# Kernel optimization log

Measured on AMD Instinct MI355X. Metric: run time of the kernel, lower is better.

Reference implementation:

```python
import jax, jax.numpy as jnp
import numpy as np

N_NODES = 100000
N_EDGES = 3200000
D_IN = 128
D_OUT = 128


def setup_inputs() -> dict:
    key = jax.random.key(0)
    k1, k2, k3 = jax.random.split(key, 3)
    x = jax.random.normal(k1, (N_NODES, D_IN), dtype=jnp.float32)
    edge_index = jax.random.randint(k2, (2, N_EDGES), 0, N_NODES, dtype=jnp.int64)
    # Glorot-style init for the GCN linear weight [out, in]
    weight = jax.random.normal(k3, (D_OUT, D_IN), dtype=jnp.float32) * (1.0 / np.sqrt(D_IN))
    bias = jnp.zeros((D_OUT,), dtype=jnp.float32)
    return {"x": x, "edge_index": edge_index, "weight": weight, "bias": bias}


def reference(x, edge_index, weight, bias):
    """LinearEncoder.forward: (GCNConv(x, edge_index), 0).

    GCNConv: out = D^-1/2 (A + I) D^-1/2 (x W^T) + b  (symmetric norm, self-loops).
    """
    n = x.shape[0]
    src = edge_index[0]
    dst = edge_index[1]
    # add self-loops
    loops = jnp.arange(n, dtype=src.dtype)
    src = jnp.concatenate([src, loops])
    dst = jnp.concatenate([dst, loops])
    # degree (in-degree over destination nodes, unit edge weights)
    ones = jnp.ones(src.shape[0], dtype=x.dtype)
    deg = jax.ops.segment_sum(ones, dst, num_segments=n)
    deg_inv_sqrt = jnp.where(deg > 0, jax.lax.rsqrt(deg), 0.0).astype(x.dtype)
    norm = deg_inv_sqrt[src] * deg_inv_sqrt[dst]  # [E+N]
    # dense transform first (as in PyG GCNConv), then sparse aggregation
    h = x @ weight.T  # [N, D_OUT]
    msgs = h[src] * norm[:, None]  # [E+N, D_OUT]
    out = jax.ops.segment_sum(msgs, dst, num_segments=n) + bias
    return (out, 0)
```

## Files before the change

### kernel.cpp

```cpp
#include <hip/hip_runtime.h>
#include <hip/hip_bf16.h>

#define N_NODES 100000
#define N_EDGES 3200000
#define D 128

typedef unsigned short u16;

#define BKT_W 512
#define NBKT 196
#define NSH 8
#define CAPS 2304
#define CAPB (NSH * CAPS)
#define EPB 5120
#define P1B 625
#define EPT 20

#define CW_BLOCKS 2

typedef __attribute__((ext_vector_type(8))) short bf16x8;
typedef __attribute__((ext_vector_type(4))) float f32x4;

__device__ __forceinline__ float bf2f(u16 u) {
    union { unsigned i; float f; } a; a.i = ((unsigned)u) << 16; return a.f;
}
__device__ __forceinline__ float asf(unsigned u) {
    union { unsigned i; float f; } a; a.i = u; return a.f;
}
__device__ __forceinline__ u16 f2bf(float f) {
    __hip_bfloat16 b = __float2bfloat16(f);
    return *(u16*)&b;
}

__global__ __launch_bounds__(256) void p1_multisplit(const int* __restrict__ ei,
                                                     int* __restrict__ bcnt,
                                                     unsigned* __restrict__ bbuf) {
    __shared__ unsigned s1[EPB];
    __shared__ unsigned s2[EPB];
    __shared__ int hist[NBKT], lbase[NBKT], cur[NBKT], gbase[NBKT];
    __shared__ int wsum4[4], wbase4[4];
    int t = threadIdx.x, blk = blockIdx.x;
    int sh = blk & (NSH - 1);
    int e0 = blk * EPB;
    if (t < NBKT) hist[t] = 0;
    __syncthreads();

    unsigned char bk[EPT];
#pragma unroll
    for (int k = 0; k < EPT; ++k) {
        int i = k * 256 + t;
        int s = ei[e0 + i];
        int d = ei[N_EDGES + e0 + i];
        unsigned bkt = (unsigned)d >> 9;
        bk[k] = (unsigned char)bkt;
        s1[i] = ((unsigned)s << 9) | ((unsigned)d & 511u);
        atomicAdd(&hist[bkt], 1);
    }
    __syncthreads();

    if (t < NBKT) gbase[t] = atomicAdd(&bcnt[t * NSH + sh], hist[t]);

    int lane = t & 63, wv = t >> 6;
    int hv = (t < NBKT) ? hist[t] : 0;
    int pre = hv;
#pragma unroll
    for (int o = 1; o < 64; o <<= 1) {
        int u = __shfl_up(pre, o);
        if (lane >= o) pre += u;
    }
    if (lane == 63) wsum4[wv] = pre;
    __syncthreads();
    if (t == 0) {
        int b = 0;
#pragma unroll
        for (int k = 0; k < 4; ++k) { wbase4[k] = b; b += wsum4[k]; }
    }
    __syncthreads();
    if (t < NBKT) { int ex = wbase4[wv] + pre - hv; lbase[t] = ex; cur[t] = ex; }
    __syncthreads();

#pragma unroll
    for (int k = 0; k < EPT; ++k) {
        int i = k * 256 + t;
        int p = atomicAdd(&cur[bk[k]], 1);
        s2[p] = s1[i];
    }
    __syncthreads();

    for (int bkt = wv; bkt < NBKT; bkt += 4) {
        int n = hist[bkt], lb = lbase[bkt], gb = gbase[bkt];
        unsigned* dst = bbuf + ((size_t)bkt * NSH + sh) * CAPS;
        for (int j = lane; j < n; j += 64) {
            int p = gb + j;
            if (p < CAPS) dst[p] = s2[lb + j];
        }
    }
}

__global__ __launch_bounds__(1024) void p2_localsort(const unsigned* __restrict__ bbuf,
                                                     const int* __restrict__ bcnt,
                                                     int* __restrict__ sorted,
                                                     int* __restrict__ beg_g,
                                                     int* __restrict__ cnt_g,
                                                     float* __restrict__ dinv_g,
                                                     const float* __restrict__ w,
                                                     u16* __restrict__ wbf) {
    __shared__ int hist[BKT_W], cur[BKT_W], shcnt[NSH];
    __shared__ int wsum[8], wbase[8];
    int b = blockIdx.x, t = threadIdx.x;

    if (b >= NBKT) {
        int idx = (b - NBKT) * 1024 + t;
        const float4* wp = (const float4*)(w + (size_t)idx * 8);
        float4 a = wp[0], bb = wp[1];
        union { u16 h[8]; uint4 v; } o;
        o.h[0] = f2bf(a.x); o.h[1] = f2bf(a.y);
        o.h[2] = f2bf(a.z); o.h[3] = f2bf(a.w);
        o.h[4] = f2bf(bb.x); o.h[5] = f2bf(bb.y);
        o.h[6] = f2bf(bb.z); o.h[7] = f2bf(bb.w);
        ((uint4*)wbf)[idx] = o.v;
        return;
    }

    if (t < NSH) { int m = bcnt[b * NSH + t]; shcnt[t] = m > CAPS ? CAPS : m; }
    if (t < BKT_W) hist[t] = 0;
    __syncthreads();

    for (int sh = 0; sh < NSH; ++sh) {
        int m = shcnt[sh];
        const unsigned* p = bbuf + ((size_t)b * NSH + sh) * CAPS;
        for (int i = t; i < m; i += 1024) atomicAdd(&hist[p[i] & 511u], 1);
    }
    __syncthreads();

    int lane = t & 63, wv = t >> 6;
    int hv = (t < BKT_W) ? hist[t] : 0;
    int pre = hv;
#pragma unroll
    for (int o = 1; o < 64; o <<= 1) {
        int u = __shfl_up(pre, o);
        if (lane >= o) pre += u;
    }
    if (wv < 8 && lane == 63) wsum[wv] = pre;
    __syncthreads();
    if (wv == 0) {
        int v = (lane < 8) ? wsum[lane] : 0;
        int pp = v;
#pragma unroll
        for (int o = 1; o < 8; o <<= 1) {
            int u = __shfl_up(pp, o);
            if (lane >= o) pp += u;
        }
        if (lane < 8) wbase[lane] = pp - v;
    }
    __syncthreads();
    int ex = 0;
    if (t < BKT_W) { ex = wbase[wv] + pre - hv; cur[t] = ex; }

    if (t < BKT_W) {
        int node = b * BKT_W + t;
        if (node < N_NODES) {
            cnt_g[node] = hv;
            beg_g[node] = b * CAPB + ex;
            dinv_g[node] = rsqrtf((float)(hv + 1));
        }
    }
    __syncthreads();

    int* dst = sorted + (size_t)b * CAPB;
    for (int sh = 0; sh < NSH; ++sh) {
        int m = shcnt[sh];
        const unsigned* p = bbuf + ((size_t)b * NSH + sh) * CAPS;
        for (int i = t; i < m; i += 1024) {
            unsigned ww = p[i];
            int pp = atomicAdd(&cur[ww & 511u], 1);
            dst[pp] = (int)(ww >> 9);
        }
    }
}

__global__ __launch_bounds__(256) void gemm_h(const float* __restrict__ x,
                                              const u16* __restrict__ wbf,
                                              const float* __restrict__ dinv,
                                              u16* __restrict__ h) {
    int t = threadIdx.x;
    int wave = t >> 6, lane = t & 63;
    int n0 = blockIdx.x * 64 + wave * 16;
    int lrow = lane & 15;
    int quad = lane >> 4;

    int arow = n0 + lrow;
    const float* ap = x + (size_t)(arow < N_NODES ? arow : 0) * D;
    bf16x8 afrag[4];
#pragma unroll
    for (int kt = 0; kt < 4; ++kt) {
        int k0 = kt * 32 + quad * 8;
        f32x4 x0 = *(const f32x4*)(ap + k0);
        f32x4 x1 = *(const f32x4*)(ap + k0 + 4);
        bf16x8 a;
        a[0] = (short)f2bf(x0.x); a[1] = (short)f2bf(x0.y);
        a[2] = (short)f2bf(x0.z); a[3] = (short)f2bf(x0.w);
        a[4] = (short)f2bf(x1.x); a[5] = (short)f2bf(x1.y);
        a[6] = (short)f2bf(x1.z); a[7] = (short)f2bf(x1.w);
        afrag[kt] = a;
    }

    float dsc[4];
#pragma unroll
    for (int i = 0; i < 4; ++i) {
        int n = n0 + quad * 4 + i;
        dsc[i] = (n < N_NODES) ? dinv[n] : 0.f;
    }

#pragma unroll
    for (int jt = 0; jt < 8; ++jt) {
        int j0 = jt * 16;
        f32x4 acc = {0.f, 0.f, 0.f, 0.f};
#pragma unroll
        for (int kt = 0; kt < 4; ++kt) {
            int k0 = kt * 32 + quad * 8;
            bf16x8 b = *(const bf16x8*)(wbf + (size_t)(j0 + lrow) * D + k0);
            acc = __builtin_amdgcn_mfma_f32_16x16x32_bf16(afrag[kt], b, acc, 0, 0, 0);
        }
#pragma unroll
        for (int i = 0; i < 4; ++i) {
            int n = n0 + quad * 4 + i;
            if (n < N_NODES) h[(size_t)n * D + j0 + lrow] = f2bf(acc[i] * dsc[i]);
        }
    }
}

__global__ __launch_bounds__(256) void aggregate_h(const u16* __restrict__ h,
                                                   const float* __restrict__ dinv,
                                                   const int* __restrict__ beg_g,
                                                   const int* __restrict__ cnt_g,
                                                   const int* __restrict__ sorted_src,
                                                   const float* __restrict__ bias,
                                                   float* __restrict__ out) {
    int w = threadIdx.x >> 6;
    int l = threadIdx.x & 63;
    int n = blockIdx.x * 4 + w;
    const unsigned* h32 = (const unsigned*)h;

    unsigned us = h32[(size_t)n * 64 + l];
    float acc0 = asf(us << 16);
    float acc1 = asf(us & 0xffff0000u);

    int c = __builtin_amdgcn_readfirstlane(cnt_g[n]);
    int beg = __builtin_amdgcn_readfirstlane(beg_g[n]);
    const int* sp = sorted_src + beg;

    int i = 0;
    for (; i + 16 <= c; i += 16) {
        int s[16];
#pragma unroll
        for (int j = 0; j < 16; ++j) s[j] = sp[i + j];
        unsigned u[16];
#pragma unroll
        for (int j = 0; j < 16; ++j) u[j] = h32[(size_t)s[j] * 64 + l];
#pragma unroll
        for (int j = 0; j < 16; ++j) {
            acc0 += asf(u[j] << 16);
            acc1 += asf(u[j] & 0xffff0000u);
        }
    }
    for (; i + 4 <= c; i += 4) {
        int s0 = sp[i], s1 = sp[i + 1], s2 = sp[i + 2], s3 = sp[i + 3];
        unsigned u0 = h32[(size_t)s0 * 64 + l];
        unsigned u1 = h32[(size_t)s1 * 64 + l];
        unsigned u2 = h32[(size_t)s2 * 64 + l];
        unsigned u3 = h32[(size_t)s3 * 64 + l];
        acc0 += asf(u0 << 16); acc1 += asf(u0 & 0xffff0000u);
        acc0 += asf(u1 << 16); acc1 += asf(u1 & 0xffff0000u);
        acc0 += asf(u2 << 16); acc1 += asf(u2 & 0xffff0000u);
        acc0 += asf(u3 << 16); acc1 += asf(u3 & 0xffff0000u);
    }
    for (; i < c; ++i) {
        unsigned u = h32[(size_t)sp[i] * 64 + l];
        acc0 += asf(u << 16); acc1 += asf(u & 0xffff0000u);
    }

    float dn = dinv[n];
    float2 bs = ((const float2*)bias)[l];
    float2 o;
    o.x = acc0 * dn + bs.x;
    o.y = acc1 * dn + bs.y;
    ((float2*)out)[(size_t)n * 64 + l] = o;

    if (blockIdx.x == 0 && threadIdx.x == 0) out[(size_t)N_NODES * D] = 0.f;
}

extern "C" void kernel_launch(void* const* d_in, const int* in_sizes, int n_in,
                              void* d_out, int out_size, void* d_ws, size_t ws_size,
                              hipStream_t stream) {
    const float* x = (const float*)d_in[0];
    const int* ei = (const int*)d_in[1];
    const float* w = (const float*)d_in[2];
    const float* bias = (const float*)d_in[3];
    float* out = (float*)d_out;

    char* ws = (char*)d_ws;
    size_t o = 0;
    auto alloc = [&](size_t bytes) -> char* {
        char* p = ws + o;
        o = (o + bytes + 511) & ~(size_t)511;
        return p;
    };
    char* regionA = alloc((size_t)N_NODES * D * 2);
    unsigned* bbuf = (unsigned*)regionA;
    u16* h = (u16*)regionA;
    int* sorted = (int*)alloc((size_t)NBKT * CAPB * 4);
    int* cnt = (int*)alloc((size_t)N_NODES * 4);
    int* beg = (int*)alloc((size_t)N_NODES * 4);
    float* dinv = (float*)alloc((size_t)N_NODES * 4);
    int* bcnt = (int*)alloc((size_t)NBKT * NSH * 4);
    u16* wbf = (u16*)alloc((size_t)D * D * 2);

    hipMemsetAsync(bcnt, 0, (size_t)NBKT * NSH * 4, stream);

    p1_multisplit<<<P1B, 256, 0, stream>>>(ei, bcnt, bbuf);
    p2_localsort<<<NBKT + CW_BLOCKS, 1024, 0, stream>>>(bbuf, bcnt, sorted, beg, cnt, dinv, w, wbf);
    gemm_h<<<(N_NODES + 63) / 64, 256, 0, stream>>>(x, wbf, dinv, h);
    aggregate_h<<<N_NODES / 4, 256, 0, stream>>>(h, dinv, beg, cnt, sorted, bias, out);
}
```

Baseline: 303.7 us.

## Store h column-blocked and aggregate per 16-column chunk for cache locality

The GEMM now writes h in a column-blocked layout (8 chunks of 16 features, each chunk contiguous across nodes). Aggregation launches one block per (32-node chunk, column chunk). Within a wave, 8 lane-groups gather different neighbors' 32-byte slices, then combine them with a shuffle reduction. The aim is to shrink the working set per column chunk (~3.2MB) so random gathers hit L2/MALL instead of HBM. The cost is that the neighbor index list is re-read 8 times, writes become 32-byte strided, and there is extra shuffle work.

```diff
diff --git a/kernel.cpp b/kernel.cpp
--- a/kernel.cpp
+++ b/kernel.cpp
@@ -17,6 +17,8 @@
 #define EPT 20
 
 #define CW_BLOCKS 2
+
+#define NCB 8
 
 typedef __attribute__((ext_vector_type(8))) short bf16x8;
 typedef __attribute__((ext_vector_type(4))) float f32x4;
@@ -225,69 +227,69 @@
 #pragma unroll
         for (int i = 0; i < 4; ++i) {
             int n = n0 + quad * 4 + i;
-            if (n < N_NODES) h[(size_t)n * D + j0 + lrow] = f2bf(acc[i] * dsc[i]);
-        }
-    }
-}
-
-__global__ __launch_bounds__(256) void aggregate_h(const u16* __restrict__ h,
-                                                   const float* __restrict__ dinv,
-                                                   const int* __restrict__ beg_g,
-                                                   const int* __restrict__ cnt_g,
-                                                   const int* __restrict__ sorted_src,
-                                                   const float* __restrict__ bias,
-                                                   float* __restrict__ out) {
-    int w = threadIdx.x >> 6;
-    int l = threadIdx.x & 63;
-    int n = blockIdx.x * 4 + w;
-    const unsigned* h32 = (const unsigned*)h;
-
-    unsigned us = h32[(size_t)n * 64 + l];
-    float acc0 = asf(us << 16);
-    float acc1 = asf(us & 0xffff0000u);
-
-    int c = __builtin_amdgcn_readfirstlane(cnt_g[n]);
-    int beg = __builtin_amdgcn_readfirstlane(beg_g[n]);
-    const int* sp = sorted_src + beg;
-
-    int i = 0;
-    for (; i + 16 <= c; i += 16) {
-        int s[16];
-#pragma unroll
-        for (int j = 0; j < 16; ++j) s[j] = sp[i + j];
-        unsigned u[16];
-#pragma unroll
-        for (int j = 0; j < 16; ++j) u[j] = h32[(size_t)s[j] * 64 + l];
-#pragma unroll
-        for (int j = 0; j < 16; ++j) {
-            acc0 += asf(u[j] << 16);
-            acc1 += asf(u[j] & 0xffff0000u);
-        }
-    }
-    for (; i + 4 <= c; i += 4) {
-        int s0 = sp[i], s1 = sp[i + 1], s2 = sp[i + 2], s3 = sp[i + 3];
-        unsigned u0 = h32[(size_t)s0 * 64 + l];
-        unsigned u1 = h32[(size_t)s1 * 64 + l];
-        unsigned u2 = h32[(size_t)s2 * 64 + l];
-        unsigned u3 = h32[(size_t)s3 * 64 + l];
-        acc0 += asf(u0 << 16); acc1 += asf(u0 & 0xffff0000u);
-        acc0 += asf(u1 << 16); acc1 += asf(u1 & 0xffff0000u);
-        acc0 += asf(u2 << 16); acc1 += asf(u2 & 0xffff0000u);
-        acc0 += asf(u3 << 16); acc1 += asf(u3 & 0xffff0000u);
-    }
-    for (; i < c; ++i) {
-        unsigned u = h32[(size_t)sp[i] * 64 + l];
-        acc0 += asf(u << 16); acc1 += asf(u & 0xffff0000u);
-    }
-
-    float dn = dinv[n];
-    float2 bs = ((const float2*)bias)[l];
-    float2 o;
-    o.x = acc0 * dn + bs.x;
-    o.y = acc1 * dn + bs.y;
-    ((float2*)out)[(size_t)n * 64 + l] = o;
-
-    if (blockIdx.x == 0 && threadIdx.x == 0) out[(size_t)N_NODES * D] = 0.f;
+            if (n < N_NODES)
+                h[((size_t)jt * N_NODES + n) * 16 + lrow] = f2bf(acc[i] * dsc[i]);
+        }
+    }
+}
+
+__global__ __launch_bounds__(256) void aggregate_cb(const u16* __restrict__ h,
+                                                    const float* __restrict__ dinv,
+                                                    const int* __restrict__ beg_g,
+                                                    const int* __restrict__ cnt_g,
+                                                    const int* __restrict__ sorted_src,
+                                                    const float* __restrict__ bias,
+                                                    float* __restrict__ out) {
+    int blk = blockIdx.x;
+    int c = blk & (NCB - 1);
+    int chunk = blk >> 3;
+    int t = threadIdx.x;
+    int wv = t >> 6, lane = t & 63;
+    int g = lane >> 3;
+    int ll = lane & 7;
+    const unsigned* hc = (const unsigned*)(h + ((size_t)c * N_NODES) * 16);
+    float2 bs = ((const float2*)bias)[c * 8 + ll];
+
+    for (int k = 0; k < 8; ++k) {
+        int n = chunk * 32 + wv * 8 + k;
+        int cn = __builtin_amdgcn_readfirstlane(cnt_g[n]);
+        int beg = __builtin_amdgcn_readfirstlane(beg_g[n]);
+        const int* sp = sorted_src + beg;
+
+        float acc0 = 0.f, acc1 = 0.f;
+        if (g == 0) {
+            unsigned u = hc[(size_t)n * 8 + ll];
+            acc0 = asf(u << 16); acc1 = asf(u & 0xffff0000u);
+        }
+        int i = 0;
+        for (; i + 16 <= cn; i += 16) {
+            int sa = __builtin_nontemporal_load(sp + i + g);
+            int sb = __builtin_nontemporal_load(sp + i + 8 + g);
+            unsigned ua = hc[(size_t)sa * 8 + ll];
+            unsigned ub = hc[(size_t)sb * 8 + ll];
+            acc0 += asf(ua << 16); acc1 += asf(ua & 0xffff0000u);
+            acc0 += asf(ub << 16); acc1 += asf(ub & 0xffff0000u);
+        }
+        for (; i < cn; i += 8) {
+            int idx = i + g;
+            if (idx < cn) {
+                int s = __builtin_nontemporal_load(sp + idx);
+                unsigned u = hc[(size_t)s * 8 + ll];
+                acc0 += asf(u << 16); acc1 += asf(u & 0xffff0000u);
+            }
+        }
+        acc0 += __shfl_xor(acc0, 8);  acc1 += __shfl_xor(acc1, 8);
+        acc0 += __shfl_xor(acc0, 16); acc1 += __shfl_xor(acc1, 16);
+        acc0 += __shfl_xor(acc0, 32); acc1 += __shfl_xor(acc1, 32);
+
+        if (g == 0) {
+            float dn = dinv[n];
+            float* op = out + (size_t)n * D + c * 16 + 2 * ll;
+            __builtin_nontemporal_store(acc0 * dn + bs.x, op);
+            __builtin_nontemporal_store(acc1 * dn + bs.y, op + 1);
+        }
+    }
+    if (blk == 0 && t == 0) out[(size_t)N_NODES * D] = 0.f;
 }
 
 extern "C" void kernel_launch(void* const* d_in, const int* in_sizes, int n_in,
@@ -321,5 +323,5 @@
     p1_multisplit<<<P1B, 256, 0, stream>>>(ei, bcnt, bbuf);
     p2_localsort<<<NBKT + CW_BLOCKS, 1024, 0, stream>>>(bbuf, bcnt, sorted, beg, cnt, dinv, w, wbf);
     gemm_h<<<(N_NODES + 63) / 64, 256, 0, stream>>>(x, wbf, dinv, h);
-    aggregate_h<<<N_NODES / 4, 256, 0, stream>>>(h, dinv, beg, cnt, sorted, bias, out);
-}
+    aggregate_cb<<<(N_NODES / 32) * NCB, 256, 0, stream>>>(h, dinv, beg, cnt, sorted, bias, out);
+}
```

After: 574.5 us. 89.1% more time.

## Fuse GEMM into edge multisplit kernel and move source normalization into aggregation

Applied to the files above, without the earlier changes.

Runs the dense x·W^T transform in extra blocks of the edge-bucketing kernel, so the GEMM no longer waits for degree computation and overlaps with the multisplit. Because dinv is not ready at GEMM time, the per-source dinv scaling moves into the aggregation loop as an extra gather per edge. p2 now stages bucket data in LDS and sorts in place into bbuf, removing the separate sorted buffer. Weight conversion becomes its own small launch. The cost is an extra dinv load per edge, larger LDS use in p2, and a larger p1 kernel footprint.

```diff
diff --git a/kernel.cpp b/kernel.cpp
--- a/kernel.cpp
+++ b/kernel.cpp
@@ -15,8 +15,7 @@
 #define EPB 5120
 #define P1B 625
 #define EPT 20
-
-#define CW_BLOCKS 2
+#define GEMM_B 1563
 
 typedef __attribute__((ext_vector_type(8))) short bf16x8;
 typedef __attribute__((ext_vector_type(4))) float f32x4;
@@ -32,14 +31,72 @@
     return *(u16*)&b;
 }
 
-__global__ __launch_bounds__(256) void p1_multisplit(const int* __restrict__ ei,
-                                                     int* __restrict__ bcnt,
-                                                     unsigned* __restrict__ bbuf) {
+__global__ __launch_bounds__(256) void wconv(const float* __restrict__ w,
+                                             u16* __restrict__ wbf) {
+    int idx = blockIdx.x * 256 + threadIdx.x;
+    const float4* wp = (const float4*)(w + (size_t)idx * 8);
+    float4 a = wp[0], bb = wp[1];
+    union { u16 h[8]; uint4 v; } o;
+    o.h[0] = f2bf(a.x); o.h[1] = f2bf(a.y);
+    o.h[2] = f2bf(a.z); o.h[3] = f2bf(a.w);
+    o.h[4] = f2bf(bb.x); o.h[5] = f2bf(bb.y);
+    o.h[6] = f2bf(bb.z); o.h[7] = f2bf(bb.w);
+    ((uint4*)wbf)[idx] = o.v;
+}
+
+__global__ __launch_bounds__(256) void p1_gemm(const int* __restrict__ ei,
+                                               int* __restrict__ bcnt,
+                                               unsigned* __restrict__ bbuf,
+                                               const float* __restrict__ x,
+                                               const u16* __restrict__ wbf,
+                                               u16* __restrict__ h) {
     __shared__ unsigned s1[EPB];
     __shared__ unsigned s2[EPB];
     __shared__ int hist[NBKT], lbase[NBKT], cur[NBKT], gbase[NBKT];
     __shared__ int wsum4[4], wbase4[4];
     int t = threadIdx.x, blk = blockIdx.x;
+
+    if (blk >= P1B) {
+        int wave = t >> 6, lane = t & 63;
+        int n0 = (blk - P1B) * 64 + wave * 16;
+        int lrow = lane & 15;
+        int quad = lane >> 4;
+
+        int arow = n0 + lrow;
+        const float* ap = x + (size_t)(arow < N_NODES ? arow : 0) * D;
+        bf16x8 afrag[4];
+#pragma unroll
+        for (int kt = 0; kt < 4; ++kt) {
+            int k0 = kt * 32 + quad * 8;
+            f32x4 x0 = *(const f32x4*)(ap + k0);
+            f32x4 x1 = *(const f32x4*)(ap + k0 + 4);
+            bf16x8 a;
+            a[0] = (short)f2bf(x0.x); a[1] = (short)f2bf(x0.y);
+            a[2] = (short)f2bf(x0.z); a[3] = (short)f2bf(x0.w);
+            a[4] = (short)f2bf(x1.x); a[5] = (short)f2bf(x1.y);
+            a[6] = (short)f2bf(x1.z); a[7] = (short)f2bf(x1.w);
+            afrag[kt] = a;
+        }
+
+#pragma unroll
+        for (int jt = 0; jt < 8; ++jt) {
+            int j0 = jt * 16;
+            f32x4 acc = {0.f, 0.f, 0.f, 0.f};
+#pragma unroll
+            for (int kt = 0; kt < 4; ++kt) {
+                int k0 = kt * 32 + quad * 8;
+                bf16x8 b = *(const bf16x8*)(wbf + (size_t)(j0 + lrow) * D + k0);
+                acc = __builtin_amdgcn_mfma_f32_16x16x32_bf16(afrag[kt], b, acc, 0, 0, 0);
+            }
+#pragma unroll
+            for (int i = 0; i < 4; ++i) {
+                int n = n0 + quad * 4 + i;
+                if (n < N_NODES) h[(size_t)n * D + j0 + lrow] = f2bf(acc[i]);
+            }
+        }
+        return;
+    }
+
     int sh = blk & (NSH - 1);
     int e0 = blk * EPB;
     if (t < NBKT) hist[t] = 0;
@@ -97,31 +154,16 @@
     }
 }
 
-__global__ __launch_bounds__(1024) void p2_localsort(const unsigned* __restrict__ bbuf,
+__global__ __launch_bounds__(1024) void p2_localsort(unsigned* __restrict__ bbuf,
                                                      const int* __restrict__ bcnt,
-                                                     int* __restrict__ sorted,
                                                      int* __restrict__ beg_g,
                                                      int* __restrict__ cnt_g,
-                                                     float* __restrict__ dinv_g,
-                                                     const float* __restrict__ w,
-                                                     u16* __restrict__ wbf) {
+                                                     float* __restrict__ dinv_g) {
+    __shared__ unsigned stage[CAPB];
     __shared__ int hist[BKT_W], cur[BKT_W], shcnt[NSH];
     __shared__ int wsum[8], wbase[8];
     int b = blockIdx.x, t = threadIdx.x;
 
-    if (b >= NBKT) {
-        int idx = (b - NBKT) * 1024 + t;
-        const float4* wp = (const float4*)(w + (size_t)idx * 8);
-        float4 a = wp[0], bb = wp[1];
-        union { u16 h[8]; uint4 v; } o;
-        o.h[0] = f2bf(a.x); o.h[1] = f2bf(a.y);
-        o.h[2] = f2bf(a.z); o.h[3] = f2bf(a.w);
-        o.h[4] = f2bf(bb.x); o.h[5] = f2bf(bb.y);
-        o.h[6] = f2bf(bb.z); o.h[7] = f2bf(bb.w);
-        ((uint4*)wbf)[idx] = o.v;
-        return;
-    }
-
     if (t < NSH) { int m = bcnt[b * NSH + t]; shcnt[t] = m > CAPS ? CAPS : m; }
     if (t < BKT_W) hist[t] = 0;
     __syncthreads();
@@ -129,7 +171,11 @@
     for (int sh = 0; sh < NSH; ++sh) {
         int m = shcnt[sh];
         const unsigned* p = bbuf + ((size_t)b * NSH + sh) * CAPS;
-        for (int i = t; i < m; i += 1024) atomicAdd(&hist[p[i] & 511u], 1);
+        for (int i = t; i < m; i += 1024) {
+            unsigned w = p[i];
+            stage[sh * CAPS + i] = w;
+            atomicAdd(&hist[w & 511u], 1);
+        }
     }
     __syncthreads();
 
@@ -167,84 +213,33 @@
     }
     __syncthreads();
 
-    int* dst = sorted + (size_t)b * CAPB;
+    int* dst = (int*)(bbuf + (size_t)b * CAPB);
     for (int sh = 0; sh < NSH; ++sh) {
         int m = shcnt[sh];
-        const unsigned* p = bbuf + ((size_t)b * NSH + sh) * CAPS;
         for (int i = t; i < m; i += 1024) {
-            unsigned ww = p[i];
+            unsigned ww = stage[sh * CAPS + i];
             int pp = atomicAdd(&cur[ww & 511u], 1);
             dst[pp] = (int)(ww >> 9);
         }
     }
 }
 
-__global__ __launch_bounds__(256) void gemm_h(const float* __restrict__ x,
-                                              const u16* __restrict__ wbf,
-                                              const float* __restrict__ dinv,
-                                              u16* __restrict__ h) {
-    int t = threadIdx.x;
-    int wave = t >> 6, lane = t & 63;
-    int n0 = blockIdx.x * 64 + wave * 16;
-    int lrow = lane & 15;
-    int quad = lane >> 4;
-
-    int arow = n0 + lrow;
-    const float* ap = x + (size_t)(arow < N_NODES ? arow : 0) * D;
-    bf16x8 afrag[4];
-#pragma unroll
-    for (int kt = 0; kt < 4; ++kt) {
-        int k0 = kt * 32 + quad * 8;
-        f32x4 x0 = *(const f32x4*)(ap + k0);
-        f32x4 x1 = *(const f32x4*)(ap + k0 + 4);
-        bf16x8 a;
-        a[0] = (short)f2bf(x0.x); a[1] = (short)f2bf(x0.y);
-        a[2] = (short)f2bf(x0.z); a[3] = (short)f2bf(x0.w);
-        a[4] = (short)f2bf(x1.x); a[5] = (short)f2bf(x1.y);
-        a[6] = (short)f2bf(x1.z); a[7] = (short)f2bf(x1.w);
-        afrag[kt] = a;
-    }
-
-    float dsc[4];
-#pragma unroll
-    for (int i = 0; i < 4; ++i) {
-        int n = n0 + quad * 4 + i;
-        dsc[i] = (n < N_NODES) ? dinv[n] : 0.f;
-    }
-
-#pragma unroll
-    for (int jt = 0; jt < 8; ++jt) {
-        int j0 = jt * 16;
-        f32x4 acc = {0.f, 0.f, 0.f, 0.f};
-#pragma unroll
-        for (int kt = 0; kt < 4; ++kt) {
-            int k0 = kt * 32 + quad * 8;
-            bf16x8 b = *(const bf16x8*)(wbf + (size_t)(j0 + lrow) * D + k0);
-            acc = __builtin_amdgcn_mfma_f32_16x16x32_bf16(afrag[kt], b, acc, 0, 0, 0);
-        }
-#pragma unroll
-        for (int i = 0; i < 4; ++i) {
-            int n = n0 + quad * 4 + i;
-            if (n < N_NODES) h[(size_t)n * D + j0 + lrow] = f2bf(acc[i] * dsc[i]);
-        }
-    }
-}
-
-__global__ __launch_bounds__(256) void aggregate_h(const u16* __restrict__ h,
-                                                   const float* __restrict__ dinv,
-                                                   const int* __restrict__ beg_g,
-                                                   const int* __restrict__ cnt_g,
-                                                   const int* __restrict__ sorted_src,
-                                                   const float* __restrict__ bias,
-                                                   float* __restrict__ out) {
+__global__ __launch_bounds__(256) void aggregate_h2(const u16* __restrict__ h,
+                                                    const float* __restrict__ dinv,
+                                                    const int* __restrict__ beg_g,
+                                                    const int* __restrict__ cnt_g,
+                                                    const int* __restrict__ sorted_src,
+                                                    const float* __restrict__ bias,
+                                                    float* __restrict__ out) {
     int w = threadIdx.x >> 6;
     int l = threadIdx.x & 63;
     int n = blockIdx.x * 4 + w;
     const unsigned* h32 = (const unsigned*)h;
 
+    float dn = dinv[n];
     unsigned us = h32[(size_t)n * 64 + l];
-    float acc0 = asf(us << 16);
-    float acc1 = asf(us & 0xffff0000u);
+    float acc0 = dn * asf(us << 16);
+    float acc1 = dn * asf(us & 0xffff0000u);
 
     int c = __builtin_amdgcn_readfirstlane(cnt_g[n]);
     int beg = __builtin_amdgcn_readfirstlane(beg_g[n]);
@@ -255,32 +250,37 @@
         int s[16];
 #pragma unroll
         for (int j = 0; j < 16; ++j) s[j] = sp[i + j];
+        float dv[16];
+#pragma unroll
+        for (int j = 0; j < 16; ++j) dv[j] = dinv[s[j]];
         unsigned u[16];
 #pragma unroll
         for (int j = 0; j < 16; ++j) u[j] = h32[(size_t)s[j] * 64 + l];
 #pragma unroll
         for (int j = 0; j < 16; ++j) {
-            acc0 += asf(u[j] << 16);
-            acc1 += asf(u[j] & 0xffff0000u);
+            acc0 += dv[j] * asf(u[j] << 16);
+            acc1 += dv[j] * asf(u[j] & 0xffff0000u);
         }
     }
     for (; i + 4 <= c; i += 4) {
         int s0 = sp[i], s1 = sp[i + 1], s2 = sp[i + 2], s3 = sp[i + 3];
+        float d0 = dinv[s0], d1 = dinv[s1], d2 = dinv[s2], d3 = dinv[s3];
         unsigned u0 = h32[(size_t)s0 * 64 + l];
         unsigned u1 = h32[(size_t)s1 * 64 + l];
         unsigned u2 = h32[(size_t)s2 * 64 + l];
         unsigned u3 = h32[(size_t)s3 * 64 + l];
-        acc0 += asf(u0 << 16); acc1 += asf(u0 & 0xffff0000u);
-        acc0 += asf(u1 << 16); acc1 += asf(u1 & 0xffff0000u);
-        acc0 += asf(u2 << 16); acc1 += asf(u2 & 0xffff0000u);
-        acc0 += asf(u3 << 16); acc1 += asf(u3 & 0xffff0000u);
+        acc0 += d0 * asf(u0 << 16); acc1 += d0 * asf(u0 & 0xffff0000u);
+        acc0 += d1 * asf(u1 << 16); acc1 += d1 * asf(u1 & 0xffff0000u);
+        acc0 += d2 * asf(u2 << 16); acc1 += d2 * asf(u2 & 0xffff0000u);
+        acc0 += d3 * asf(u3 << 16); acc1 += d3 * asf(u3 & 0xffff0000u);
     }
     for (; i < c; ++i) {
-        unsigned u = h32[(size_t)sp[i] * 64 + l];
-        acc0 += asf(u << 16); acc1 += asf(u & 0xffff0000u);
-    }
-
-    float dn = dinv[n];
+        int s = sp[i];
+        float dv = dinv[s];
+        unsigned u = h32[(size_t)s * 64 + l];
+        acc0 += dv * asf(u << 16); acc1 += dv * asf(u & 0xffff0000u);
+    }
+
     float2 bs = ((const float2*)bias)[l];
     float2 o;
     o.x = acc0 * dn + bs.x;
@@ -306,10 +306,9 @@
         o = (o + bytes + 511) & ~(size_t)511;
         return p;
     };
-    char* regionA = alloc((size_t)N_NODES * D * 2);
-    unsigned* bbuf = (unsigned*)regionA;
-    u16* h = (u16*)regionA;
-    int* sorted = (int*)alloc((size_t)NBKT * CAPB * 4);
+    u16* h = (u16*)alloc((size_t)N_NODES * D * 2);
+    unsigned* bbuf = (unsigned*)alloc((size_t)NBKT * CAPB * 4);
+    int* sorted = (int*)bbuf;
     int* cnt = (int*)alloc((size_t)N_NODES * 4);
     int* beg = (int*)alloc((size_t)N_NODES * 4);
     float* dinv = (float*)alloc((size_t)N_NODES * 4);
@@ -318,8 +317,8 @@
 
     hipMemsetAsync(bcnt, 0, (size_t)NBKT * NSH * 4, stream);
 
-    p1_multisplit<<<P1B, 256, 0, stream>>>(ei, bcnt, bbuf);
-    p2_localsort<<<NBKT + CW_BLOCKS, 1024, 0, stream>>>(bbuf, bcnt, sorted, beg, cnt, dinv, w, wbf);
-    gemm_h<<<(N_NODES + 63) / 64, 256, 0, stream>>>(x, wbf, dinv, h);
-    aggregate_h<<<N_NODES / 4, 256, 0, stream>>>(h, dinv, beg, cnt, sorted, bias, out);
-}
+    wconv<<<8, 256, 0, stream>>>(w, wbf);
+    p1_gemm<<<P1B + GEMM_B, 256, 0, stream>>>(ei, bcnt, bbuf, x, wbf, h);
+    p2_localsort<<<NBKT, 1024, 0, stream>>>(bbuf, bcnt, beg, cnt, dinv);
+    aggregate_h2<<<N_NODES / 4, 256, 0, stream>>>(h, dinv, beg, cnt, sorted, bias, out);
+}
```

New measurement: 294.4 us. -3.1%, faster.
